# Optimization experiments

Hardware: AMD Instinct MI355X
Metric: run time of the kernel (lower is better)

Reference implementation:

```python
import jax, jax.numpy as jnp
import numpy as np


def _conv1x1(W, b, x):
    # 1x1 conv == per-pixel matmul over channels: (O,C) x (B,C,H,W) -> (B,O,H,W)
    return jnp.einsum('oc,bchw->bohw', W, x) + b[None, :, None, None]


def setup_inputs() -> dict:
    key = jax.random.key(0)
    ks = jax.random.split(key, 7)
    B, C, H, W = 4, 256, 64, 64
    Cq = C // 8  # 32
    scale_qk = 1.0 / np.sqrt(C)
    x = jax.random.normal(ks[0], (B, C, H, W), dtype=jnp.float32)
    Wq = jax.random.normal(ks[1], (Cq, C), dtype=jnp.float32) * scale_qk
    bq = jnp.zeros((Cq,), dtype=jnp.float32)
    Wk = jax.random.normal(ks[2], (Cq, C), dtype=jnp.float32) * scale_qk
    bk = jnp.zeros((Cq,), dtype=jnp.float32)
    Wv = jax.random.normal(ks[3], (C, C), dtype=jnp.float32) * scale_qk
    bv = jnp.zeros((C,), dtype=jnp.float32)
    gamma = jnp.ones((1,), dtype=jnp.float32)  # torch init is 0; use 1 so attn branch is exercised
    return {'x': x, 'Wq': Wq, 'bq': bq, 'Wk': Wk, 'bk': bk, 'Wv': Wv, 'bv': bv, 'gamma': gamma}


def reference(x, Wq, bq, Wk, bk, Wv, bv, gamma):
    B, C, H, W = x.shape
    N = H * W
    # query/key projections + activation (relu), flattened over spatial dims
    q = jax.nn.relu(_conv1x1(Wq, bq, x)).reshape(B, -1, N)  # (B, C/8, N)
    k = jax.nn.relu(_conv1x1(Wk, bk, x)).reshape(B, -1, N)  # (B, C/8, N)
    # energy[b,n,m] = sum_c q[b,c,n] * k[b,c,m]  (= proj_query^T @ proj_key)
    energy = jnp.einsum('bcn,bcm->bnm', q, k)               # (B, N, N)
    attention = jax.nn.softmax(energy, axis=-1)
    v = jax.nn.relu(_conv1x1(Wv, bv, x)).reshape(B, C, N)   # (B, C, N)
    # out = v @ attention^T : out[b,c,n] = sum_m v[b,c,m] * attention[b,n,m]
    out = jnp.einsum('bcm,bnm->bcn', v, attention).reshape(B, C, H, W)
    out = gamma[0] * out + x
    return (out, attention)
```

## Files before the change

### kernel.cpp

```cpp
#include <hip/hip_runtime.h>
#include <hip/hip_bf16.h>

#define NB 4
#define NC 256
#define NQ 32
#define NN 4096
#define LOG2E 1.4426950408889634f
#define SHIFT 44.0f

typedef __attribute__((ext_vector_type(4))) float f32x4;
typedef __attribute__((ext_vector_type(8))) short s16x8;

#define MFMA16(a, b, c) __builtin_amdgcn_mfma_f32_16x16x32_bf16((a), (b), (c), 0, 0, 0)

__device__ __forceinline__ float fexp2(float x) {
    float r;
    asm("v_exp_f32 %0, %1" : "=v"(r) : "v"(x));
    return r;
}

__device__ __forceinline__ void block_sync_lds() {
    asm volatile("s_waitcnt lgkmcnt(0)" ::: "memory");
    __builtin_amdgcn_s_barrier();
}

__device__ __forceinline__ int pswz(int row, int col) {
    return row * 64 + (col ^ ((row & 7) << 3));
}

__global__ __launch_bounds__(512, 3) void k_proj(
    const float* __restrict__ x,
    const float* __restrict__ Wq, const float* __restrict__ bq,
    const float* __restrict__ Wk, const float* __restrict__ bk,
    const float* __restrict__ Wv, const float* __restrict__ bv,
    __hip_bfloat16* __restrict__ qh, __hip_bfloat16* __restrict__ ql,
    __hip_bfloat16* __restrict__ kh, __hip_bfloat16* __restrict__ kl,
    __hip_bfloat16* __restrict__ vo)
{
    __shared__ __align__(16) float xs[NC * 32];
    const int b  = blockIdx.y;
    const int n0 = blockIdx.x * 32;
    const int t  = threadIdx.x;

    {
        const float* xb = x + (size_t)b * NC * NN + n0;
        #pragma unroll
        for (int it = 0; it < 4; ++it) {
            int i4 = t + it * 512;
            int c  = i4 >> 3;
            int nq = (i4 & 7) << 2;
            float4 v4 = *(const float4*)(xb + (size_t)c * NN + nq);
            *(float4*)&xs[c * 32 + nq] = v4;
        }
    }
    __syncthreads();

    const int g  = t >> 3;
    const int n4 = (t & 7) << 2;

    const float* Wr[5];
    float a[5][4];
    #pragma unroll
    for (int j = 0; j < 5; ++j) {
        int o = g + 64 * j;
        const float* Wrow; float bias;
        if (o < 32)      { Wrow = Wq + o * NC;        bias = bq[o]; }
        else if (o < 64) { Wrow = Wk + (o - 32) * NC; bias = bk[o - 32]; }
        else             { Wrow = Wv + (o - 64) * NC; bias = bv[o - 64]; }
        Wr[j] = Wrow;
        a[j][0] = a[j][1] = a[j][2] = a[j][3] = bias;
    }

    #pragma unroll 2
    for (int c0 = 0; c0 < NC; c0 += 4) {
        float4 xv[4];
        #pragma unroll
        for (int i = 0; i < 4; ++i) xv[i] = *(const float4*)&xs[(c0 + i) * 32 + n4];
        #pragma unroll
        for (int j = 0; j < 5; ++j) {
            float4 w = *(const float4*)(Wr[j] + c0);
            a[j][0] += w.x * xv[0].x + w.y * xv[1].x + w.z * xv[2].x + w.w * xv[3].x;
            a[j][1] += w.x * xv[0].y + w.y * xv[1].y + w.z * xv[2].y + w.w * xv[3].y;
            a[j][2] += w.x * xv[0].z + w.y * xv[1].z + w.z * xv[2].z + w.w * xv[3].z;
            a[j][3] += w.x * xv[0].w + w.y * xv[1].w + w.z * xv[2].w + w.w * xv[3].w;
        }
    }

    #pragma unroll
    for (int j = 0; j < 5; ++j) {
        int o = g + 64 * j;
        float a0 = fmaxf(a[j][0], 0.f), a1 = fmaxf(a[j][1], 0.f);
        float a2 = fmaxf(a[j][2], 0.f), a3 = fmaxf(a[j][3], 0.f);
        int nn = n0 + n4;
        if (o < 64) {
            __hip_bfloat16 *dh, *dl; int c; float sc;
            if (o < 32) { dh = qh; dl = ql; c = o;      sc = LOG2E; }
            else        { dh = kh; dl = kl; c = o - 32; sc = 1.0f;  }
            float vals[4] = {a0 * sc, a1 * sc, a2 * sc, a3 * sc};
            #pragma unroll
            for (int i = 0; i < 4; ++i) {
                float vv = vals[i];
                __hip_bfloat16 h = __float2bfloat16(vv);
                float lo = vv - __bfloat162float(h);
                size_t base = ((size_t)b * NN + nn + i) * NQ + c;
                dh[base] = h;
                dl[base] = __float2bfloat16(lo);
            }
        } else {
            union { __hip_bfloat16 h[4]; unsigned long long u; } pk;
            pk.h[0] = __float2bfloat16(a0); pk.h[1] = __float2bfloat16(a1);
            pk.h[2] = __float2bfloat16(a2); pk.h[3] = __float2bfloat16(a3);
            *(unsigned long long*)(vo + ((size_t)b * NC + (o - 64)) * NN + nn) = pk.u;
        }
    }
}

__global__ __launch_bounds__(512, 3) void k_fused(
    const __hip_bfloat16* __restrict__ qh, const __hip_bfloat16* __restrict__ ql,
    const __hip_bfloat16* __restrict__ kh, const __hip_bfloat16* __restrict__ kl,
    const __hip_bfloat16* __restrict__ v,
    const float* __restrict__ x, const float* __restrict__ gamma,
    float* __restrict__ out, float* __restrict__ att)
{
    __shared__ __align__(16) __hip_bfloat16 ps[2][32 * 64];
    __shared__ float redS[8][16];
    __shared__ float finI[32];

    const int bid  = blockIdx.x;
    const int swzb = (bid & 7) * 64 + (bid >> 3);
    const int b    = swzb >> 7;
    const int n0   = (swzb & 127) * 32;

    const int t = threadIdx.x, wv = t >> 6, lane = t & 63;
    const int r = lane & 15, hi = lane >> 4, kc = hi * 8;
    const int hi4 = hi * 4;
    const int nt = wv >> 2, mt = wv & 3, mt16 = mt * 16;

    const __hip_bfloat16* khb = kh + (size_t)b * NN * NQ;
    const __hip_bfloat16* klb = kl + (size_t)b * NN * NQ;
    const __hip_bfloat16* vb  = v  + (size_t)b * NC * NN;

    const s16x8 aqh = *(const s16x8*)(qh + ((size_t)b * NN + n0 + nt * 16 + r) * NQ + kc);
    const s16x8 aql = *(const s16x8*)(ql + ((size_t)b * NN + n0 + nt * 16 + r) * NQ + kc);

    {
        const int mb = mt * 1024;
        float S = 0.f;
        s16x8 c0h = *(const s16x8*)(khb + (size_t)(mb + r) * NQ + kc);
        s16x8 c0l = *(const s16x8*)(klb + (size_t)(mb + r) * NQ + kc);
        s16x8 c1h = *(const s16x8*)(khb + (size_t)(mb + 16 + r) * NQ + kc);
        s16x8 c1l = *(const s16x8*)(klb + (size_t)(mb + 16 + r) * NQ + kc);
        #pragma unroll 1
        for (int it = 0; it < 32; ++it) {
            s16x8 u0h = c0h, u0l = c0l, u1h = c1h, u1l = c1l;
            if (it < 31) {
                int m = mb + (it + 1) * 32;
                c0h = *(const s16x8*)(khb + (size_t)(m + r) * NQ + kc);
                c0l = *(const s16x8*)(klb + (size_t)(m + r) * NQ + kc);
                c1h = *(const s16x8*)(khb + (size_t)(m + 16 + r) * NQ + kc);
                c1l = *(const s16x8*)(klb + (size_t)(m + 16 + r) * NQ + kc);
            }
            f32x4 e0 = {0.f, 0.f, 0.f, 0.f}, e1 = {0.f, 0.f, 0.f, 0.f};
            e0 = MFMA16(u0h, aqh, e0); e0 = MFMA16(u0l, aqh, e0); e0 = MFMA16(u0h, aql, e0);
            e1 = MFMA16(u1h, aqh, e1); e1 = MFMA16(u1l, aqh, e1); e1 = MFMA16(u1h, aql, e1);
            S += fexp2(e0[0] - SHIFT) + fexp2(e0[1] - SHIFT) +
                 fexp2(e0[2] - SHIFT) + fexp2(e0[3] - SHIFT) +
                 fexp2(e1[0] - SHIFT) + fexp2(e1[1] - SHIFT) +
                 fexp2(e1[2] - SHIFT) + fexp2(e1[3] - SHIFT);
        }
        S += __shfl_xor(S, 16);
        S += __shfl_xor(S, 32);
        if (lane < 16) redS[wv][r] = S;
    }
    __syncthreads();
    if (t < 32) {
        const int g4 = (t >> 4) * 4, tl = t & 15;
        finI[t] = 1.0f / (redS[g4][tl] + redS[g4 + 1][tl] +
                          redS[g4 + 2][tl] + redS[g4 + 3][tl]);
    }
    __syncthreads();

    const float fI = finI[nt * 16 + r];
    float* arow = att + ((size_t)b * NN + n0 + nt * 16 + r) * NN;
    const __hip_bfloat16* vr0 = vb + (size_t)(wv * 32 + r) * NN;
    const __hip_bfloat16* vr1 = vb + (size_t)(wv * 32 + 16 + r) * NN;

    f32x4 acc[2][2] = {};
    s16x8 kA[2], kB[2], VA[2][2], VB[2][2];

    kA[0] = *(const s16x8*)(khb + (size_t)(mt16 + r) * NQ + kc);
    kA[1] = *(const s16x8*)(klb + (size_t)(mt16 + r) * NQ + kc);
    #pragma unroll
    for (int ks = 0; ks < 2; ++ks) {
        VA[0][ks] = *(const s16x8*)(vr0 + ks * 32 + kc);
        VA[1][ks] = *(const s16x8*)(vr1 + ks * 32 + kc);
    }

    auto sub = [&](int s, s16x8 (&kC)[2], s16x8 (&kN)[2],
                   s16x8 (&VC)[2][2], s16x8 (&VN)[2][2]) {
        const int m0 = s * 64;
        if (s < 63) {
            const int mn = m0 + 64;
            kN[0] = *(const s16x8*)(khb + (size_t)(mn + mt16 + r) * NQ + kc);
            kN[1] = *(const s16x8*)(klb + (size_t)(mn + mt16 + r) * NQ + kc);
            #pragma unroll
            for (int ks = 0; ks < 2; ++ks) {
                VN[0][ks] = *(const s16x8*)(vr0 + mn + ks * 32 + kc);
                VN[1][ks] = *(const s16x8*)(vr1 + mn + ks * 32 + kc);
            }
        }
        f32x4 e = {0.f, 0.f, 0.f, 0.f};
        e = MFMA16(kC[0], aqh, e); e = MFMA16(kC[1], aqh, e); e = MFMA16(kC[0], aql, e);
        f32x4 p;
        #pragma unroll
        for (int j = 0; j < 4; ++j) p[j] = fexp2(e[j] - SHIFT) * fI;
        __builtin_nontemporal_store(p, (f32x4*)(arow + m0 + mt16 + hi4));
        union { __hip_bfloat16 h[4]; unsigned long long u; } pk;
        #pragma unroll
        for (int j = 0; j < 4; ++j) pk.h[j] = __float2bfloat16(p[j]);
        *(unsigned long long*)&ps[s & 1][pswz(nt * 16 + r, mt16 + hi4)] = pk.u;

        block_sync_lds();

        #pragma unroll
        for (int nt2 = 0; nt2 < 2; ++nt2) {
            s16x8 pf0 = *(const s16x8*)&ps[s & 1][pswz(nt2 * 16 + r, kc)];
            s16x8 pf1 = *(const s16x8*)&ps[s & 1][pswz(nt2 * 16 + r, 32 + kc)];
            __builtin_amdgcn_s_setprio(1);
            acc[0][nt2] = MFMA16(VC[0][0], pf0, acc[0][nt2]);
            acc[0][nt2] = MFMA16(VC[0][1], pf1, acc[0][nt2]);
            acc[1][nt2] = MFMA16(VC[1][0], pf0, acc[1][nt2]);
            acc[1][nt2] = MFMA16(VC[1][1], pf1, acc[1][nt2]);
            __builtin_amdgcn_s_setprio(0);
        }
    };

    #pragma unroll 1
    for (int it = 0; it < 32; ++it) {
        sub(2 * it,     kA, kB, VA, VB);
        sub(2 * it + 1, kB, kA, VB, VA);
    }

    const float gm = gamma[0];
    #pragma unroll
    for (int ct = 0; ct < 2; ++ct) {
        #pragma unroll
        for (int nt2 = 0; nt2 < 2; ++nt2) {
            #pragma unroll
            for (int j = 0; j < 4; ++j) {
                int c = wv * 32 + ct * 16 + hi4 + j;
                size_t idx = ((size_t)b * NC + c) * NN + n0 + nt2 * 16 + r;
                out[idx] = gm * acc[ct][nt2][j] + x[idx];
            }
        }
    }
}

extern "C" void kernel_launch(void* const* d_in, const int* in_sizes, int n_in,
                              void* d_out, int out_size, void* d_ws, size_t ws_size,
                              hipStream_t stream) {
    const float* x     = (const float*)d_in[0];
    const float* Wq    = (const float*)d_in[1];
    const float* bq    = (const float*)d_in[2];
    const float* Wk    = (const float*)d_in[3];
    const float* bk    = (const float*)d_in[4];
    const float* Wv    = (const float*)d_in[5];
    const float* bv    = (const float*)d_in[6];
    const float* gamma = (const float*)d_in[7];

    float* out = (float*)d_out;
    float* att = out + (size_t)NB * NC * NN;

    const size_t qk_elems = (size_t)NB * NN * NQ;
    __hip_bfloat16* qh = (__hip_bfloat16*)d_ws;
    __hip_bfloat16* ql = qh + qk_elems;
    __hip_bfloat16* kh = ql + qk_elems;
    __hip_bfloat16* kl = kh + qk_elems;
    __hip_bfloat16* vo = kl + qk_elems;

    k_proj <<<dim3(NN / 32, NB), 512, 0, stream>>>(x, Wq, bq, Wk, bk, Wv, bv,
                                                   qh, ql, kh, kl, vo);
    k_fused<<<dim3(512), 512, 0, stream>>>(qh, ql, kh, kl, vo,
                                           x, gamma, out, att);
}
```

Measured before the change: 237.7 us.

## Keep P in registers and drop LDS exchange in fused attention kernel

The fused kernel moves from 8 to 4 waves per block. Each wave now computes the full 32-query by 32-key energy tile itself, using a permuted key-row mapping so the MFMA output layout feeds directly as the B operand of the PV MFMA. This removes the shared-memory P buffer and the per-step block barrier. In exchange, each wave recomputes QK for all 32 queries (4x the QK MFMAs), keeps more registers live, and the block has fewer threads for latency hiding.

```diff
diff --git a/kernel.cpp b/kernel.cpp
--- a/kernel.cpp
+++ b/kernel.cpp
@@ -17,15 +17,6 @@
     float r;
     asm("v_exp_f32 %0, %1" : "=v"(r) : "v"(x));
     return r;
-}
-
-__device__ __forceinline__ void block_sync_lds() {
-    asm volatile("s_waitcnt lgkmcnt(0)" ::: "memory");
-    __builtin_amdgcn_s_barrier();
-}
-
-__device__ __forceinline__ int pswz(int row, int col) {
-    return row * 64 + (col ^ ((row & 7) << 3));
 }
 
 __global__ __launch_bounds__(512, 3) void k_proj(
@@ -115,45 +106,44 @@
     }
 }
 
-__global__ __launch_bounds__(512, 3) void k_fused(
+__global__ __launch_bounds__(256, 2) void k_fused(
     const __hip_bfloat16* __restrict__ qh, const __hip_bfloat16* __restrict__ ql,
     const __hip_bfloat16* __restrict__ kh, const __hip_bfloat16* __restrict__ kl,
     const __hip_bfloat16* __restrict__ v,
     const float* __restrict__ x, const float* __restrict__ gamma,
     float* __restrict__ out, float* __restrict__ att)
 {
-    __shared__ __align__(16) __hip_bfloat16 ps[2][32 * 64];
-    __shared__ float redS[8][16];
+    __shared__ float redS[4][16];
     __shared__ float finI[32];
 
     const int bid  = blockIdx.x;
-    const int swzb = (bid & 7) * 64 + (bid >> 3);
-    const int b    = swzb >> 7;
-    const int n0   = (swzb & 127) * 32;
+    const int flat = (bid & 7) * 64 + (bid >> 3);
+    const int b    = flat >> 7;
+    const int n0   = (flat & 127) * 32;
 
     const int t = threadIdx.x, wv = t >> 6, lane = t & 63;
-    const int r = lane & 15, hi = lane >> 4, kc = hi * 8;
-    const int hi4 = hi * 4;
-    const int nt = wv >> 2, mt = wv & 3, mt16 = mt * 16;
+    const int r = lane & 15, hi = lane >> 4, kc = hi * 8, h8 = hi * 8;
 
     const __hip_bfloat16* khb = kh + (size_t)b * NN * NQ;
     const __hip_bfloat16* klb = kl + (size_t)b * NN * NQ;
     const __hip_bfloat16* vb  = v  + (size_t)b * NC * NN;
-
-    const s16x8 aqh = *(const s16x8*)(qh + ((size_t)b * NN + n0 + nt * 16 + r) * NQ + kc);
-    const s16x8 aql = *(const s16x8*)(ql + ((size_t)b * NN + n0 + nt * 16 + r) * NQ + kc);
+    const __hip_bfloat16* qhb = qh + ((size_t)b * NN + n0) * NQ;
+    const __hip_bfloat16* qlb = ql + ((size_t)b * NN + n0) * NQ;
 
     {
-        const int mb = mt * 1024;
+        const int rs = wv & 1, mh = wv >> 1;
+        const s16x8 aqh = *(const s16x8*)(qhb + (size_t)(rs * 16 + r) * NQ + kc);
+        const s16x8 aql = *(const s16x8*)(qlb + (size_t)(rs * 16 + r) * NQ + kc);
+        const int mb = mh * 2048;
         float S = 0.f;
         s16x8 c0h = *(const s16x8*)(khb + (size_t)(mb + r) * NQ + kc);
         s16x8 c0l = *(const s16x8*)(klb + (size_t)(mb + r) * NQ + kc);
         s16x8 c1h = *(const s16x8*)(khb + (size_t)(mb + 16 + r) * NQ + kc);
         s16x8 c1l = *(const s16x8*)(klb + (size_t)(mb + 16 + r) * NQ + kc);
         #pragma unroll 1
-        for (int it = 0; it < 32; ++it) {
+        for (int it = 0; it < 64; ++it) {
             s16x8 u0h = c0h, u0l = c0l, u1h = c1h, u1l = c1l;
-            if (it < 31) {
+            if (it < 63) {
                 int m = mb + (it + 1) * 32;
                 c0h = *(const s16x8*)(khb + (size_t)(m + r) * NQ + kc);
                 c0l = *(const s16x8*)(klb + (size_t)(m + r) * NQ + kc);
@@ -174,83 +164,102 @@
     }
     __syncthreads();
     if (t < 32) {
-        const int g4 = (t >> 4) * 4, tl = t & 15;
-        finI[t] = 1.0f / (redS[g4][tl] + redS[g4 + 1][tl] +
-                          redS[g4 + 2][tl] + redS[g4 + 3][tl]);
+        const int rs = t >> 4, tl = t & 15;
+        finI[t] = 1.0f / (redS[rs][tl] + redS[2 + rs][tl]);
     }
     __syncthreads();
 
-    const float fI = finI[nt * 16 + r];
-    float* arow = att + ((size_t)b * NN + n0 + nt * 16 + r) * NN;
-    const __hip_bfloat16* vr0 = vb + (size_t)(wv * 32 + r) * NN;
-    const __hip_bfloat16* vr1 = vb + (size_t)(wv * 32 + 16 + r) * NN;
-
-    f32x4 acc[2][2] = {};
-    s16x8 kA[2], kB[2], VA[2][2], VB[2][2];
-
-    kA[0] = *(const s16x8*)(khb + (size_t)(mt16 + r) * NQ + kc);
-    kA[1] = *(const s16x8*)(klb + (size_t)(mt16 + r) * NQ + kc);
-    #pragma unroll
-    for (int ks = 0; ks < 2; ++ks) {
-        VA[0][ks] = *(const s16x8*)(vr0 + ks * 32 + kc);
-        VA[1][ks] = *(const s16x8*)(vr1 + ks * 32 + kc);
-    }
-
-    auto sub = [&](int s, s16x8 (&kC)[2], s16x8 (&kN)[2],
-                   s16x8 (&VC)[2][2], s16x8 (&VN)[2][2]) {
-        const int m0 = s * 64;
-        if (s < 63) {
-            const int mn = m0 + 64;
-            kN[0] = *(const s16x8*)(khb + (size_t)(mn + mt16 + r) * NQ + kc);
-            kN[1] = *(const s16x8*)(klb + (size_t)(mn + mt16 + r) * NQ + kc);
-            #pragma unroll
-            for (int ks = 0; ks < 2; ++ks) {
-                VN[0][ks] = *(const s16x8*)(vr0 + mn + ks * 32 + kc);
-                VN[1][ks] = *(const s16x8*)(vr1 + mn + ks * 32 + kc);
-            }
-        }
-        f32x4 e = {0.f, 0.f, 0.f, 0.f};
-        e = MFMA16(kC[0], aqh, e); e = MFMA16(kC[1], aqh, e); e = MFMA16(kC[0], aql, e);
-        f32x4 p;
-        #pragma unroll
-        for (int j = 0; j < 4; ++j) p[j] = fexp2(e[j] - SHIFT) * fI;
-        __builtin_nontemporal_store(p, (f32x4*)(arow + m0 + mt16 + hi4));
-        union { __hip_bfloat16 h[4]; unsigned long long u; } pk;
-        #pragma unroll
-        for (int j = 0; j < 4; ++j) pk.h[j] = __float2bfloat16(p[j]);
-        *(unsigned long long*)&ps[s & 1][pswz(nt * 16 + r, mt16 + hi4)] = pk.u;
-
-        block_sync_lds();
-
-        #pragma unroll
-        for (int nt2 = 0; nt2 < 2; ++nt2) {
-            s16x8 pf0 = *(const s16x8*)&ps[s & 1][pswz(nt2 * 16 + r, kc)];
-            s16x8 pf1 = *(const s16x8*)&ps[s & 1][pswz(nt2 * 16 + r, 32 + kc)];
-            __builtin_amdgcn_s_setprio(1);
-            acc[0][nt2] = MFMA16(VC[0][0], pf0, acc[0][nt2]);
-            acc[0][nt2] = MFMA16(VC[0][1], pf1, acc[0][nt2]);
-            acc[1][nt2] = MFMA16(VC[1][0], pf0, acc[1][nt2]);
-            acc[1][nt2] = MFMA16(VC[1][1], pf1, acc[1][nt2]);
-            __builtin_amdgcn_s_setprio(0);
-        }
+    const int cw = wv * 64;
+    const s16x8 aqh0 = *(const s16x8*)(qhb + (size_t)(r) * NQ + kc);
+    const s16x8 aql0 = *(const s16x8*)(qlb + (size_t)(r) * NQ + kc);
+    const s16x8 aqh1 = *(const s16x8*)(qhb + (size_t)(16 + r) * NQ + kc);
+    const s16x8 aql1 = *(const s16x8*)(qlb + (size_t)(16 + r) * NQ + kc);
+    const float fI0 = finI[r], fI1 = finI[16 + r];
+
+    float* arow0 = att + ((size_t)b * NN + n0 + r) * NN;
+    float* arow1 = arow0 + (size_t)16 * NN;
+
+    const int p0r = ((r >> 2) << 3) | (r & 3);
+    const __hip_bfloat16* kh0 = khb + (size_t)p0r * NQ + kc;
+    const __hip_bfloat16* kl0 = klb + (size_t)p0r * NQ + kc;
+    const __hip_bfloat16* kh1 = khb + (size_t)(p0r + 4) * NQ + kc;
+    const __hip_bfloat16* kl1 = klb + (size_t)(p0r + 4) * NQ + kc;
+    const __hip_bfloat16* vr0 = vb + (size_t)(cw + r) * NN + kc;
+    const __hip_bfloat16* vr1 = vb + (size_t)(cw + 16 + r) * NN + kc;
+    const __hip_bfloat16* vr2 = vb + (size_t)(cw + 32 + r) * NN + kc;
+    const __hip_bfloat16* vr3 = vb + (size_t)(cw + 48 + r) * NN + kc;
+
+    f32x4 acc[4][2] = {};
+    s16x8 kA[4], kB[4], vA[4], vB[4];
+
+    kA[0] = *(const s16x8*)(kh0); kA[1] = *(const s16x8*)(kl0);
+    kA[2] = *(const s16x8*)(kh1); kA[3] = *(const s16x8*)(kl1);
+    vA[0] = *(const s16x8*)(vr0); vA[1] = *(const s16x8*)(vr1);
+    vA[2] = *(const s16x8*)(vr2); vA[3] = *(const s16x8*)(vr3);
+
+    auto sub = [&](int s, s16x8 (&kC)[4], s16x8 (&kN)[4],
+                   s16x8 (&vC)[4], s16x8 (&vN)[4]) {
+        const int m0 = s * 32;
+        if (s < 127) {
+            const size_t mo = (size_t)(m0 + 32) * NQ;
+            kN[0] = *(const s16x8*)(kh0 + mo); kN[1] = *(const s16x8*)(kl0 + mo);
+            kN[2] = *(const s16x8*)(kh1 + mo); kN[3] = *(const s16x8*)(kl1 + mo);
+            vN[0] = *(const s16x8*)(vr0 + m0 + 32); vN[1] = *(const s16x8*)(vr1 + m0 + 32);
+            vN[2] = *(const s16x8*)(vr2 + m0 + 32); vN[3] = *(const s16x8*)(vr3 + m0 + 32);
+        }
+        f32x4 e00 = {0.f,0.f,0.f,0.f}, e01 = {0.f,0.f,0.f,0.f};
+        f32x4 e10 = {0.f,0.f,0.f,0.f}, e11 = {0.f,0.f,0.f,0.f};
+        e00 = MFMA16(kC[0], aqh0, e00); e00 = MFMA16(kC[1], aqh0, e00); e00 = MFMA16(kC[0], aql0, e00);
+        e01 = MFMA16(kC[2], aqh0, e01); e01 = MFMA16(kC[3], aqh0, e01); e01 = MFMA16(kC[2], aql0, e01);
+        e10 = MFMA16(kC[0], aqh1, e10); e10 = MFMA16(kC[1], aqh1, e10); e10 = MFMA16(kC[0], aql1, e10);
+        e11 = MFMA16(kC[2], aqh1, e11); e11 = MFMA16(kC[3], aqh1, e11); e11 = MFMA16(kC[2], aql1, e11);
+
+        f32x4 p00, p01, p10, p11;
+        #pragma unroll
+        for (int j = 0; j < 4; ++j) {
+            p00[j] = fexp2(e00[j] - SHIFT) * fI0;
+            p01[j] = fexp2(e01[j] - SHIFT) * fI0;
+            p10[j] = fexp2(e10[j] - SHIFT) * fI1;
+            p11[j] = fexp2(e11[j] - SHIFT) * fI1;
+        }
+        __builtin_nontemporal_store(p00, (f32x4*)(arow0 + m0 + h8));
+        __builtin_nontemporal_store(p01, (f32x4*)(arow0 + m0 + h8 + 4));
+        __builtin_nontemporal_store(p10, (f32x4*)(arow1 + m0 + h8));
+        __builtin_nontemporal_store(p11, (f32x4*)(arow1 + m0 + h8 + 4));
+        union { short s[8]; s16x8 v; } u0, u1;
+        #pragma unroll
+        for (int j = 0; j < 4; ++j) {
+            u0.s[j]     = (short)__bfloat16_as_ushort(__float2bfloat16(p00[j]));
+            u0.s[4 + j] = (short)__bfloat16_as_ushort(__float2bfloat16(p01[j]));
+            u1.s[j]     = (short)__bfloat16_as_ushort(__float2bfloat16(p10[j]));
+            u1.s[4 + j] = (short)__bfloat16_as_ushort(__float2bfloat16(p11[j]));
+        }
+        acc[0][0] = MFMA16(vC[0], u0.v, acc[0][0]);
+        acc[1][0] = MFMA16(vC[1], u0.v, acc[1][0]);
+        acc[2][0] = MFMA16(vC[2], u0.v, acc[2][0]);
+        acc[3][0] = MFMA16(vC[3], u0.v, acc[3][0]);
+        acc[0][1] = MFMA16(vC[0], u1.v, acc[0][1]);
+        acc[1][1] = MFMA16(vC[1], u1.v, acc[1][1]);
+        acc[2][1] = MFMA16(vC[2], u1.v, acc[2][1]);
+        acc[3][1] = MFMA16(vC[3], u1.v, acc[3][1]);
     };
 
     #pragma unroll 1
-    for (int it = 0; it < 32; ++it) {
-        sub(2 * it,     kA, kB, VA, VB);
-        sub(2 * it + 1, kB, kA, VB, VA);
+    for (int it = 0; it < 64; ++it) {
+        sub(2 * it,     kA, kB, vA, vB);
+        sub(2 * it + 1, kB, kA, vB, vA);
     }
 
     const float gm = gamma[0];
     #pragma unroll
-    for (int ct = 0; ct < 2; ++ct) {
-        #pragma unroll
-        for (int nt2 = 0; nt2 < 2; ++nt2) {
+    for (int cc = 0; cc < 4; ++cc) {
+        #pragma unroll
+        for (int ns = 0; ns < 2; ++ns) {
             #pragma unroll
             for (int j = 0; j < 4; ++j) {
-                int c = wv * 32 + ct * 16 + hi4 + j;
-                size_t idx = ((size_t)b * NC + c) * NN + n0 + nt2 * 16 + r;
-                out[idx] = gm * acc[ct][nt2][j] + x[idx];
+                int c = cw + cc * 16 + hi * 4 + j;
+                size_t idx = ((size_t)b * NC + c) * NN + n0 + ns * 16 + r;
+                out[idx] = gm * acc[cc][ns][j] + x[idx];
             }
         }
     }
@@ -280,6 +289,6 @@
 
     k_proj <<<dim3(NN / 32, NB), 512, 0, stream>>>(x, Wq, bq, Wk, bk, Wv, bv,
                                                    qh, ql, kh, kl, vo);
-    k_fused<<<dim3(512), 512, 0, stream>>>(qh, ql, kh, kl, vo,
+    k_fused<<<dim3(512), 256, 0, stream>>>(qh, ql, kh, kl, vo,
                                            x, gamma, out, att);
 }
```

Result: slower. 361.9 us (+52.2%).
